# Kernel optimization log

Measured on AMD Instinct MI355X. Metric: run time of the kernel, lower is better.

## Reference

```python
import jax, jax.numpy as jnp
import numpy as np

# Matches the torch constant: 1/sqrt(2*3.14159) (NOT math.pi)
INV_SQRT_2PI = 1.0 / np.sqrt(np.float32(2.0 * 3.14159))


def density_ir_normal(x):
    return INV_SQRT_2PI * jnp.exp(-0.5 * x * x)


def setup_inputs() -> dict:
    key = jax.random.key(0)
    k1, k2, k3 = jax.random.split(key, 3)
    batch = 8388608           # 2**23 output slots
    n_events = 16777216       # 2**24 scattered events (avg 2 per slot)
    idx = jax.random.randint(k1, (n_events,), 0, batch)
    vals = jax.random.normal(k2, (n_events,), dtype=jnp.float32)
    # theta0 in (0,1) (branch prob), theta1 > 0 (scale), theta2 (loc)
    thetas = jnp.array([0.7, 1.3, 0.2], dtype=jnp.float32)
    return {"batch": batch, "idx": idx, "vals": vals, "thetas": thetas}


def reference(batch, idx, vals, thetas):
    # l_4_high = min(thetas[0], 1); l_5 = max(l_4_high, 0) -> clip(theta0, 0, 1)
    l_5_lhs_integral = jnp.clip(thetas[0], 0.0, 1.0)
    l_1_cond = 1.0 - l_5_lhs_integral
    # per-event multiplicative factor (vectorized density evaluation)
    z = (vals - thetas[2]) / thetas[1]
    factors = (1.0 - l_1_cond) * density_ir_normal(z) / thetas[1]
    # multiplicative scatter; duplicate indices multiply in (matches the
    # sequential result[idx[i]] *= factor loop, product is order-invariant)
    result = jnp.ones(batch, dtype=vals.dtype).at[idx].multiply(factors)
    return result * l_1_cond
```

## Files before the change

kernel.cpp:

```cpp
#include <hip/hip_runtime.h>
#include <climits>


#define INV_SQRT_2PI 0.39894246f
#define SLOT_BITS 14
#define SLOTS (1 << SLOT_BITS)
#define NB_MAX 512
#define NBLK 512
#define BTHREADS 512
#define TILE 2048
#define STAGE_S 28
#define QSCALE 8192.0f
#define QMASK 0x3FFFFu

__device__ __forceinline__ long long region_idx(int blk, int b, int nbuckets,
                                                int swzmask) {
    int bb = swzmask ? ((b + blk) & swzmask) : b;
    return (long long)blk * nbuckets + bb;
}

__device__ __forceinline__ void ovf_push(uint2* ovf, int* ovf_cnt, int ovcap,
                                         unsigned gslot, unsigned q) {
    int op = atomicAdd(ovf_cnt, 1);
    if (op < ovcap) ovf[op] = make_uint2(gslot, q);
}

struct Ev4 { int4 k; float4 v; int cnt; };

__device__ __forceinline__ Ev4 load4(const int* __restrict__ idx,
                                     const float* __restrict__ vals,
                                     long long base, long long te) {
    Ev4 r; r.cnt = 0;
    r.k = make_int4(0,0,0,0); r.v = make_float4(0,0,0,0);
    if (base + 4 <= te) {
        r.k = *(const int4*)(idx + base);
        r.v = *(const float4*)(vals + base);
        r.cnt = 4;
    } else if (base < te) {
        int c = (int)(te - base);
        int kk[4] = {0,0,0,0}; float vv[4] = {0,0,0,0};
        for (int i = 0; i < c; ++i) { kk[i] = idx[base+i]; vv[i] = vals[base+i]; }
        r.k = make_int4(kk[0],kk[1],kk[2],kk[3]);
        r.v = make_float4(vv[0],vv[1],vv[2],vv[3]);
        r.cnt = c;
    }
    return r;
}

__global__ __launch_bounds__(BTHREADS) void bin_kernel(
        const int* __restrict__ idx, const float* __restrict__ vals,
        const float* __restrict__ thetas,
        unsigned* __restrict__ pairs,
        int* __restrict__ fill,
        uint2* __restrict__ ovf, int* __restrict__ ovf_cnt, int ovcap,
        int n, int nbuckets, int cap_shift, int swzmask, int epb) {
    __shared__ unsigned stage[NB_MAX * STAGE_S];
    __shared__ int scnt[NB_MAX];
    __shared__ int cnum[NB_MAX];

    const int tid = threadIdx.x;
    const int blk = blockIdx.x;
    const int cappb = 1 << cap_shift;
    long long start = (long long)blk * epb;
    long long end = start + epb;
    if (end > n) end = n;

    for (int b = tid; b < nbuckets; b += BTHREADS) { scnt[b] = 0; cnum[b] = 0; }
    __syncthreads();

    const float t1 = thetas[1], t2 = thetas[2];
    const float t0c = fminf(fmaxf(thetas[0], 0.0f), 1.0f);
    const float inv_t1 = 1.0f / t1;

    Ev4 cur; cur.cnt = 0;
    if (start < end) {
        long long te0 = start + TILE; if (te0 > end) te0 = end;
        cur = load4(idx, vals, start + (long long)tid * 4, te0);
    }

    for (long long ts = start; ts < end; ts += TILE) {
        Ev4 nxt; nxt.cnt = 0;
        long long tsn = ts + TILE;
        if (tsn < end) {
            long long ten = tsn + TILE; if (ten > end) ten = end;
            nxt = load4(idx, vals, tsn + (long long)tid * 4, ten);
        }

        int   kk[4] = {cur.k.x, cur.k.y, cur.k.z, cur.k.w};
        float vv[4] = {cur.v.x, cur.v.y, cur.v.z, cur.v.w};
        int bs[4]; unsigned recs[4]; int pos[4];
        #pragma unroll
        for (int j = 0; j < 4; ++j) {
            unsigned uk = (unsigned)kk[j];
            bs[j] = (int)(uk >> SLOT_BITS);
            float z = (vv[j] - t2) * inv_t1;
            float u = 0.5f * z * z;
            unsigned q = __float2uint_rn(fminf(u * QSCALE, (float)QMASK));
            recs[j] = ((uk & (SLOTS - 1)) << 18) | q;
        }
        #pragma unroll
        for (int j = 0; j < 4; ++j) {
            pos[j] = (j < cur.cnt && bs[j] < nbuckets)
                     ? atomicAdd(&scnt[bs[j]], 1) : INT_MAX;
        }
        #pragma unroll
        for (int j = 0; j < 4; ++j) {
            if (pos[j] == INT_MAX) continue;
            if (pos[j] < STAGE_S) stage[bs[j] * STAGE_S + pos[j]] = recs[j];
            else ovf_push(ovf, ovf_cnt, ovcap, (unsigned)kk[j], recs[j] & QMASK);
        }
        __syncthreads();

        for (int b = tid; b < nbuckets; b += BTHREADS) {
            int c = scnt[b]; if (c > STAGE_S) c = STAGE_S;
            if (c >= 16) {
                int have = cnum[b];
                if (have < (cappb >> 4)) {
                    unsigned* dst = pairs +
                        (region_idx(blk, b, nbuckets, swzmask) << cap_shift) + (have << 4);
                    const uint4* s4 = (const uint4*)&stage[b * STAGE_S];
                    uint4* d4 = (uint4*)dst;
                    d4[0]=s4[0]; d4[1]=s4[1]; d4[2]=s4[2]; d4[3]=s4[3];
                    cnum[b] = have + 1;
                    int rem = c - 16;
                    for (int i = 0; i < rem; ++i)
                        stage[b*STAGE_S + i] = stage[b*STAGE_S + 16 + i];
                    scnt[b] = rem;
                } else {
                    for (int i = 0; i < c; ++i) {
                        unsigned r = stage[b*STAGE_S + i];
                        ovf_push(ovf, ovf_cnt, ovcap,
                                 ((unsigned)b << SLOT_BITS) | (r >> 18), r & QMASK);
                    }
                    scnt[b] = 0;
                }
            } else scnt[b] = c;
        }
        __syncthreads();
        cur = nxt;
    }

    for (int b = tid; b < nbuckets; b += BTHREADS) {
        int c = scnt[b]; if (c > STAGE_S) c = STAGE_S;
        int have = cnum[b];
        int valid = have << 4;
        int nfull = (c + 15) >> 4;
        int fit = (cappb >> 4) - have;
        int nw = nfull < fit ? nfull : fit;
        if (nw > 0) {
            unsigned* dst = pairs +
                (region_idx(blk, b, nbuckets, swzmask) << cap_shift) + (have << 4);
            const uint4* s4 = (const uint4*)&stage[b * STAGE_S];
            uint4* d4 = (uint4*)dst;
            for (int ch = 0; ch < nw; ++ch) {
                d4[ch*4+0]=s4[ch*4+0]; d4[ch*4+1]=s4[ch*4+1];
                d4[ch*4+2]=s4[ch*4+2]; d4[ch*4+3]=s4[ch*4+3];
            }
            int v2 = nw << 4; if (v2 > c) v2 = c;
            valid += v2;
        }
        for (int i = (nw << 4); i < c; ++i) {
            unsigned r = stage[b*STAGE_S + i];
            ovf_push(ovf, ovf_cnt, ovcap,
                     ((unsigned)b << SLOT_BITS) | (r >> 18), r & QMASK);
        }
        fill[region_idx(blk, b, nbuckets, swzmask)] = valid;
    }
}

__global__ __launch_bounds__(1024) void reduce_kernel(
        const unsigned* __restrict__ pairs, const int* __restrict__ fill,
        const uint2* __restrict__ ovf, const int* __restrict__ ovf_cnt, int ovcap,
        const float* __restrict__ thetas, float* __restrict__ out,
        long long n_out, int nbuckets, int cap_shift, int swzmask) {
    __shared__ unsigned accu[SLOTS];
    const int tid = threadIdx.x;
    const int b = blockIdx.x;

    for (int s = tid; s < SLOTS; s += 1024) accu[s] = 0u;
    __syncthreads();

    const int wave = tid >> 6, lane = tid & 63;
    const int SEGS = NBLK / 16;

    int sl = wave + (lane & 31) * 16;
    int cntv = fill[region_idx(sl, b, nbuckets, swzmask)];

    const unsigned* pc = pairs +
        (region_idx(wave, b, nbuckets, swzmask) << cap_shift);
    unsigned a0 = pc[lane];
    unsigned a1 = pc[64 + lane];

    for (int i = 0; i < SEGS; ++i) {
        const unsigned* pn = pc; unsigned n0 = 0, n1 = 0;
        if (i < SEGS - 1) {
            int sn = wave + (i + 1) * 16;
            pn = pairs + (region_idx(sn, b, nbuckets, swzmask) << cap_shift);
            n0 = pn[lane];
            n1 = pn[64 + lane];
        }
        int ca = __builtin_amdgcn_readlane(cntv, i);
        if (lane < ca)      atomicAdd(&accu[a0 >> 18], (1u << 25) + (a0 & QMASK));
        if (64 + lane < ca) atomicAdd(&accu[a1 >> 18], (1u << 25) + (a1 & QMASK));
        for (int r = 128 + lane; r < ca; r += 64) {
            unsigned rec = pc[r];
            atomicAdd(&accu[rec >> 18], (1u << 25) + (rec & QMASK));
        }
        pc = pn; a0 = n0; a1 = n1;
    }
    __syncthreads();

    int no = *ovf_cnt; if (no > ovcap) no = ovcap;
    for (int i = tid; i < no; i += 1024) {
        uint2 e = ovf[i];
        if ((int)(e.x >> SLOT_BITS) == b)
            atomicAdd(&accu[e.x & (SLOTS - 1)], (1u << 25) + e.y);
    }
    __syncthreads();

    const float t1 = thetas[1];
    const float t0c = fminf(fmaxf(thetas[0], 0.0f), 1.0f);
    const float logC = logf(t0c * INV_SQRT_2PI / t1);
    const float cond = 1.0f - t0c;
    long long obase = (long long)b << SLOT_BITS;
    for (int ss = tid; ss < SLOTS; ss += 1024) {
        long long o = obase + ss;
        if (o < n_out) {
            unsigned av = accu[ss];
            float v = (float)(av >> 25) * logC
                    - (float)(av & 0x1FFFFFFu) * (1.0f / QSCALE);
            out[o] = cond * expf(v);
        }
    }
}

__global__ void init_zero_kernel(float* __restrict__ out, int n) {
    int i = blockIdx.x * blockDim.x + threadIdx.x;
    int stride = gridDim.x * blockDim.x;
    for (; i < n; i += stride) out[i] = 0.0f;
}
__global__ void scatter_log_kernel(const int* __restrict__ idx,
                                   const float* __restrict__ vals,
                                   const float* __restrict__ thetas,
                                   float* __restrict__ acc, int n) {
    float t1 = thetas[1], t2 = thetas[2];
    float t0c = fminf(fmaxf(thetas[0], 0.0f), 1.0f);
    float logC = logf(t0c * INV_SQRT_2PI / t1);
    float inv_t1 = 1.0f / t1;
    int i = blockIdx.x * blockDim.x + threadIdx.x;
    int stride = gridDim.x * blockDim.x;
    for (; i < n; i += stride) {
        float z = (vals[i] - t2) * inv_t1;
        atomicAdd(&acc[idx[i]], fmaf(-0.5f * z, z, logC));
    }
}
__global__ void finalize_kernel(float* __restrict__ out,
                                const float* __restrict__ thetas, int n) {
    float t0c = fminf(fmaxf(thetas[0], 0.0f), 1.0f);
    float cond = 1.0f - t0c;
    int i = blockIdx.x * blockDim.x + threadIdx.x;
    int stride = gridDim.x * blockDim.x;
    for (; i < n; i += stride) out[i] = cond * expf(out[i]);
}

extern "C" void kernel_launch(void* const* d_in, const int* in_sizes, int n_in,
                              void* d_out, int out_size, void* d_ws, size_t ws_size,
                              hipStream_t stream) {
    const int*   idx    = (const int*)d_in[1];
    const float* vals   = (const float*)d_in[2];
    const float* thetas = (const float*)d_in[3];
    float*       out    = (float*)d_out;

    int n_events = in_sizes[1];
    long long n_out = out_size;
    int nbuckets = (int)((n_out + SLOTS - 1) >> SLOT_BITS);

    long long tiles_total = ((long long)n_events + TILE - 1) / TILE;
    long long tpb = (tiles_total + NBLK - 1) / NBLK;
    int epb = (int)(tpb * TILE);
    long long avg = nbuckets > 0 ? (epb + nbuckets - 1) / nbuckets : 1;
    long long want = avg + avg / 2 + 32;
    int cap_shift = 6;
    while ((1LL << cap_shift) < want && cap_shift < 20) ++cap_shift;
    long long cappb = 1LL << cap_shift;
    int swzmask = (nbuckets > 0 && (nbuckets & (nbuckets - 1)) == 0)
                  ? nbuckets - 1 : 0;

    size_t pairs_b = (size_t)NBLK * nbuckets * cappb * 4;
    size_t fill_b  = (size_t)NBLK * nbuckets * 4;
    size_t head    = pairs_b + fill_b + 64;
    bool fast = (nbuckets > 0) && (nbuckets <= NB_MAX) && (n_events > 0) &&
                (ws_size >= head + 64 * 1024);

    if (fast) {
        unsigned* pairs = (unsigned*)d_ws;
        int* fill = (int*)((char*)d_ws + pairs_b);
        int* ovf_cnt = (int*)((char*)d_ws + pairs_b + fill_b);
        uint2* ovf = (uint2*)((char*)d_ws + head);
        long long ovcap_ll = (long long)((ws_size - head) / 8);
        int ovcap = (int)(ovcap_ll > 4194304 ? 4194304 : ovcap_ll);

        hipMemsetAsync(ovf_cnt, 0, sizeof(int), stream);
        bin_kernel<<<NBLK, BTHREADS, 0, stream>>>(idx, vals, thetas, pairs, fill,
                                                  ovf, ovf_cnt, ovcap,
                                                  n_events, nbuckets, cap_shift,
                                                  swzmask, epb);
        reduce_kernel<<<nbuckets, 1024, 0, stream>>>(pairs, fill, ovf, ovf_cnt,
                                                     ovcap, thetas, out,
                                                     n_out, nbuckets, cap_shift,
                                                     swzmask);
    } else {
        const int BLOCK = 256;
        int grid_out = min((int)((n_out + BLOCK - 1) / BLOCK), 2048);
        int grid_ev  = min((n_events + BLOCK - 1) / BLOCK, 2048);
        init_zero_kernel<<<grid_out, BLOCK, 0, stream>>>(out, (int)n_out);
        scatter_log_kernel<<<grid_ev, BLOCK, 0, stream>>>(idx, vals, thetas, out, n_events);
        finalize_kernel<<<grid_out, BLOCK, 0, stream>>>(out, thetas, (int)n_out);
    }
}
```

Before: 100.4 us.

## Write binned records directly to global regions instead of LDS staging

Removes the shared-memory staging buffer, the per-tile syncthreads and the 16-record chunked flushes in the binning kernel. Each event now takes a slot from the per-bucket LDS atomic counter and writes its packed record straight into that block's global bucket region, spilling to the overflow list once capacity is reached. This drops two barriers per tile and the LDS copy traffic, but turns the coalesced 64-byte chunk writes into scattered 4-byte global stores and loses the explicit next-tile prefetch.

```diff
diff --git a/kernel.cpp b/kernel.cpp
--- a/kernel.cpp
+++ b/kernel.cpp
@@ -8,8 +8,6 @@
 #define NB_MAX 512
 #define NBLK 512
 #define BTHREADS 512
-#define TILE 2048
-#define STAGE_S 28
 #define QSCALE 8192.0f
 #define QMASK 0x3FFFFu
 
@@ -23,28 +21,6 @@
                                          unsigned gslot, unsigned q) {
     int op = atomicAdd(ovf_cnt, 1);
     if (op < ovcap) ovf[op] = make_uint2(gslot, q);
-}
-
-struct Ev4 { int4 k; float4 v; int cnt; };
-
-__device__ __forceinline__ Ev4 load4(const int* __restrict__ idx,
-                                     const float* __restrict__ vals,
-                                     long long base, long long te) {
-    Ev4 r; r.cnt = 0;
-    r.k = make_int4(0,0,0,0); r.v = make_float4(0,0,0,0);
-    if (base + 4 <= te) {
-        r.k = *(const int4*)(idx + base);
-        r.v = *(const float4*)(vals + base);
-        r.cnt = 4;
-    } else if (base < te) {
-        int c = (int)(te - base);
-        int kk[4] = {0,0,0,0}; float vv[4] = {0,0,0,0};
-        for (int i = 0; i < c; ++i) { kk[i] = idx[base+i]; vv[i] = vals[base+i]; }
-        r.k = make_int4(kk[0],kk[1],kk[2],kk[3]);
-        r.v = make_float4(vv[0],vv[1],vv[2],vv[3]);
-        r.cnt = c;
-    }
-    return r;
 }
 
 __global__ __launch_bounds__(BTHREADS) void bin_kernel(
@@ -54,40 +30,38 @@
         int* __restrict__ fill,
         uint2* __restrict__ ovf, int* __restrict__ ovf_cnt, int ovcap,
         int n, int nbuckets, int cap_shift, int swzmask, int epb) {
-    __shared__ unsigned stage[NB_MAX * STAGE_S];
     __shared__ int scnt[NB_MAX];
-    __shared__ int cnum[NB_MAX];
 
     const int tid = threadIdx.x;
     const int blk = blockIdx.x;
-    const int cappb = 1 << cap_shift;
+    const int cap = 1 << cap_shift;
     long long start = (long long)blk * epb;
     long long end = start + epb;
     if (end > n) end = n;
 
-    for (int b = tid; b < nbuckets; b += BTHREADS) { scnt[b] = 0; cnum[b] = 0; }
+    for (int b = tid; b < nbuckets; b += BTHREADS) scnt[b] = 0;
     __syncthreads();
 
     const float t1 = thetas[1], t2 = thetas[2];
     const float t0c = fminf(fmaxf(thetas[0], 0.0f), 1.0f);
     const float inv_t1 = 1.0f / t1;
 
-    Ev4 cur; cur.cnt = 0;
-    if (start < end) {
-        long long te0 = start + TILE; if (te0 > end) te0 = end;
-        cur = load4(idx, vals, start + (long long)tid * 4, te0);
-    }
-
-    for (long long ts = start; ts < end; ts += TILE) {
-        Ev4 nxt; nxt.cnt = 0;
-        long long tsn = ts + TILE;
-        if (tsn < end) {
-            long long ten = tsn + TILE; if (ten > end) ten = end;
-            nxt = load4(idx, vals, tsn + (long long)tid * 4, ten);
-        }
-
-        int   kk[4] = {cur.k.x, cur.k.y, cur.k.z, cur.k.w};
-        float vv[4] = {cur.v.x, cur.v.y, cur.v.z, cur.v.w};
+    for (long long base = start + (long long)tid * 4; base < end;
+         base += (long long)BTHREADS * 4) {
+        int   kk[4]; float vv[4]; int cnt;
+        if (base + 4 <= end) {
+            int4   k4 = *(const int4*)(idx + base);
+            float4 v4 = *(const float4*)(vals + base);
+            kk[0]=k4.x; kk[1]=k4.y; kk[2]=k4.z; kk[3]=k4.w;
+            vv[0]=v4.x; vv[1]=v4.y; vv[2]=v4.z; vv[3]=v4.w;
+            cnt = 4;
+        } else {
+            cnt = (int)(end - base);
+            #pragma unroll
+            for (int i = 0; i < 4; ++i) { kk[i] = 0; vv[i] = 0.0f; }
+            for (int i = 0; i < cnt; ++i) { kk[i] = idx[base+i]; vv[i] = vals[base+i]; }
+        }
+
         int bs[4]; unsigned recs[4]; int pos[4];
         #pragma unroll
         for (int j = 0; j < 4; ++j) {
@@ -100,71 +74,24 @@
         }
         #pragma unroll
         for (int j = 0; j < 4; ++j) {
-            pos[j] = (j < cur.cnt && bs[j] < nbuckets)
+            pos[j] = (j < cnt && bs[j] < nbuckets)
                      ? atomicAdd(&scnt[bs[j]], 1) : INT_MAX;
         }
         #pragma unroll
         for (int j = 0; j < 4; ++j) {
             if (pos[j] == INT_MAX) continue;
-            if (pos[j] < STAGE_S) stage[bs[j] * STAGE_S + pos[j]] = recs[j];
-            else ovf_push(ovf, ovf_cnt, ovcap, (unsigned)kk[j], recs[j] & QMASK);
-        }
-        __syncthreads();
-
-        for (int b = tid; b < nbuckets; b += BTHREADS) {
-            int c = scnt[b]; if (c > STAGE_S) c = STAGE_S;
-            if (c >= 16) {
-                int have = cnum[b];
-                if (have < (cappb >> 4)) {
-                    unsigned* dst = pairs +
-                        (region_idx(blk, b, nbuckets, swzmask) << cap_shift) + (have << 4);
-                    const uint4* s4 = (const uint4*)&stage[b * STAGE_S];
-                    uint4* d4 = (uint4*)dst;
-                    d4[0]=s4[0]; d4[1]=s4[1]; d4[2]=s4[2]; d4[3]=s4[3];
-                    cnum[b] = have + 1;
-                    int rem = c - 16;
-                    for (int i = 0; i < rem; ++i)
-                        stage[b*STAGE_S + i] = stage[b*STAGE_S + 16 + i];
-                    scnt[b] = rem;
-                } else {
-                    for (int i = 0; i < c; ++i) {
-                        unsigned r = stage[b*STAGE_S + i];
-                        ovf_push(ovf, ovf_cnt, ovcap,
-                                 ((unsigned)b << SLOT_BITS) | (r >> 18), r & QMASK);
-                    }
-                    scnt[b] = 0;
-                }
-            } else scnt[b] = c;
-        }
-        __syncthreads();
-        cur = nxt;
-    }
-
+            if (pos[j] < cap)
+                pairs[(region_idx(blk, bs[j], nbuckets, swzmask) << cap_shift)
+                      + pos[j]] = recs[j];
+            else
+                ovf_push(ovf, ovf_cnt, ovcap, (unsigned)kk[j], recs[j] & QMASK);
+        }
+    }
+
+    __syncthreads();
     for (int b = tid; b < nbuckets; b += BTHREADS) {
-        int c = scnt[b]; if (c > STAGE_S) c = STAGE_S;
-        int have = cnum[b];
-        int valid = have << 4;
-        int nfull = (c + 15) >> 4;
-        int fit = (cappb >> 4) - have;
-        int nw = nfull < fit ? nfull : fit;
-        if (nw > 0) {
-            unsigned* dst = pairs +
-                (region_idx(blk, b, nbuckets, swzmask) << cap_shift) + (have << 4);
-            const uint4* s4 = (const uint4*)&stage[b * STAGE_S];
-            uint4* d4 = (uint4*)dst;
-            for (int ch = 0; ch < nw; ++ch) {
-                d4[ch*4+0]=s4[ch*4+0]; d4[ch*4+1]=s4[ch*4+1];
-                d4[ch*4+2]=s4[ch*4+2]; d4[ch*4+3]=s4[ch*4+3];
-            }
-            int v2 = nw << 4; if (v2 > c) v2 = c;
-            valid += v2;
-        }
-        for (int i = (nw << 4); i < c; ++i) {
-            unsigned r = stage[b*STAGE_S + i];
-            ovf_push(ovf, ovf_cnt, ovcap,
-                     ((unsigned)b << SLOT_BITS) | (r >> 18), r & QMASK);
-        }
-        fill[region_idx(blk, b, nbuckets, swzmask)] = valid;
+        int c = scnt[b]; if (c > cap) c = cap;
+        fill[region_idx(blk, b, nbuckets, swzmask)] = c;
     }
 }
 
@@ -275,9 +202,8 @@
     long long n_out = out_size;
     int nbuckets = (int)((n_out + SLOTS - 1) >> SLOT_BITS);
 
-    long long tiles_total = ((long long)n_events + TILE - 1) / TILE;
-    long long tpb = (tiles_total + NBLK - 1) / NBLK;
-    int epb = (int)(tpb * TILE);
+    long long epb_ll = (((long long)n_events + NBLK - 1) / NBLK + 2047) & ~2047LL;
+    int epb = (int)epb_ll;
     long long avg = nbuckets > 0 ? (epb + nbuckets - 1) / nbuckets : 1;
     long long want = avg + avg / 2 + 32;
     int cap_shift = 6;
```

After: 278.4 us. 177% more time.
